# Kernel optimization log

Hardware: AMD Instinct MI355X
Metric: run time of the kernel (lower is better)

The kernel has to match this reference:

```python
import jax, jax.numpy as jnp
import numpy as np

DIM_V, DIM_T, DIM_OUT, NUM_HEADS = 1024, 1024, 1024, 16
HEAD_DIM = DIM_OUT // NUM_HEADS
BETA = 1.0  # module multiplies scores by self.beta (=1); self.scale is unused


def setup_inputs() -> dict:
    key = jax.random.key(0)
    ks = jax.random.split(key, 12)
    B, N1, N2 = 8, 256, 4096
    E = jax.random.normal(ks[0], (B, N1, DIM_T), dtype=jnp.float32)
    I = jax.random.normal(ks[1], (B, N2, DIM_V), dtype=jnp.float32)
    s = 0.02
    # Conv1d(kernel_size=1) == linear; weights stored [out, in], bias [out]
    q_w = jax.random.normal(ks[2], (DIM_OUT, DIM_T), dtype=jnp.float32) * s
    q_b = jnp.zeros((DIM_OUT,), dtype=jnp.float32)
    k_w = jax.random.normal(ks[3], (DIM_OUT, DIM_V), dtype=jnp.float32) * s
    k_b = jnp.zeros((DIM_OUT,), dtype=jnp.float32)
    v_w = jax.random.normal(ks[4], (DIM_OUT, DIM_V), dtype=jnp.float32) * s
    v_b = jnp.zeros((DIM_OUT,), dtype=jnp.float32)
    p_w = jax.random.normal(ks[5], (DIM_OUT, DIM_OUT), dtype=jnp.float32) * s
    p_b = jnp.zeros((DIM_OUT,), dtype=jnp.float32)
    return {"E": E, "I": I, "q_w": q_w, "q_b": q_b, "k_w": k_w, "k_b": k_b,
            "v_w": v_w, "v_b": v_b, "p_w": p_w, "p_b": p_b}


def reference(E, I, q_w, q_b, k_w, k_b, v_w, v_b, p_w, p_b):
    B, N1, _ = E.shape
    _, N2, _ = I.shape
    # 1x1 conv projections == dense layers over channel dim
    Q = (jnp.einsum('bnc,oc->bno', E, q_w) + q_b).reshape(B, N1, NUM_HEADS, HEAD_DIM)
    K = (jnp.einsum('bmc,oc->bmo', I, k_w) + k_b).reshape(B, N2, NUM_HEADS, HEAD_DIM)
    V = (jnp.einsum('bmc,oc->bmo', I, v_w) + v_b).reshape(B, N2, NUM_HEADS, HEAD_DIM)
    # cross-attention scores [B, H, N1, N2]
    attn = jnp.einsum('bnhd,bmhd->bhnm', Q, K) * BETA
    attn = jax.nn.softmax(attn, axis=-1)
    U = jnp.einsum('bhnm,bmhd->bnhd', attn, V).reshape(B, N1, DIM_OUT)
    U = jnp.einsum('bnc,oc->bno', U, p_w) + p_b
    U = U / jnp.linalg.norm(U, axis=-1, keepdims=True)
    return jnp.concatenate([E, U], axis=2)  # [B, N1, dim_t + dim_out]
```

## Files before the change

### kernel.cpp

```cpp
#include <hip/hip_runtime.h>
#include <hip/hip_bf16.h>
#include <stdint.h>


typedef __bf16 bf16_t;
typedef __attribute__((ext_vector_type(8))) __bf16 bf16x8;
typedef __attribute__((ext_vector_type(4))) float f32x4;

#define DEVINL __device__ __forceinline__

DEVINL f32x4 mfma16(bf16x8 a, bf16x8 b, f32x4 c) {
  return __builtin_amdgcn_mfma_f32_16x16x32_bf16(a, b, c, 0, 0, 0);
}

DEVINL bf16x8 load8(const bf16_t* p) { return *(const bf16x8*)p; }
DEVINL bf16x8 load8(const float* p) {
  const float4 u = *(const float4*)p;
  const float4 v = *(const float4*)(p + 4);
  bf16x8 r;
  r[0] = (bf16_t)u.x; r[1] = (bf16_t)u.y; r[2] = (bf16_t)u.z; r[3] = (bf16_t)u.w;
  r[4] = (bf16_t)v.x; r[5] = (bf16_t)v.y; r[6] = (bf16_t)v.z; r[7] = (bf16_t)v.w;
  return r;
}

DEVINL uint32_t pack_bf16(float a, float b) {
  union { bf16_t h[2]; uint32_t u; } x;
  x.h[0] = (bf16_t)a; x.h[1] = (bf16_t)b;
  return x.u;
}

DEVINL void async16(const void* g, void* l) {
  typedef const __attribute__((address_space(1))) unsigned int* gp1;
  typedef __attribute__((address_space(3))) unsigned int* lp3;
  __builtin_amdgcn_global_load_lds((gp1)(uintptr_t)g,
                                   (lp3)(uint32_t)(uintptr_t)l, 16, 0, 0);
}

__global__ __launch_bounds__(256) void cvt_f32_bf16(
    const float* __restrict__ src, bf16_t* __restrict__ dst, int n8) {
  const int i = blockIdx.x * 256 + threadIdx.x;
  if (i < n8) *(bf16x8*)(dst + (size_t)i * 8) = load8(src + (size_t)i * 8);
}

template <int MODE>
__global__ __launch_bounds__(256) void gemm_bt_async(
    const bf16_t* __restrict__ A, const bf16_t* __restrict__ B,
    const float* __restrict__ bias, bf16_t* __restrict__ C,
    int M, int N, int K) {
  __shared__ bf16_t As[2][128 * 32];
  __shared__ bf16_t Bs[2][128 * 32];
  const int tid = threadIdx.x;
  const int w = tid >> 6, lane = tid & 63, quad = lane >> 4, l16 = lane & 15;
  const int bid = blockIdx.x;
  const int swz = (bid & 7) * (int)(gridDim.x >> 3) + (bid >> 3);
  const int big = swz >> 3, small = swz & 7;
  const int bm = 128 * (MODE == 1 ? small : big);
  const int bn = 128 * (MODE == 1 ? big : small);
  const int wm = (w & 1) * 64, wn = (w >> 1) * 64;
  const int srow = tid >> 2;
  const int sw8 = ((tid & 3) ^ (srow & 3)) * 8;

  const bf16_t* Ag0 = A + (size_t)(bm + srow) * K + sw8;
  const bf16_t* Ag1 = Ag0 + (size_t)64 * K;
  const bf16_t* Bg0 = B + (size_t)(bn + srow) * K + sw8;
  const bf16_t* Bg1 = Bg0 + (size_t)64 * K;

  f32x4 acc[4][4] = {};

  for (int k0 = 0; k0 < K; k0 += 64) {
    async16(Ag0 + k0, As[0] + tid * 8);
    async16(Ag1 + k0, As[0] + 64 * 32 + tid * 8);
    async16(Bg0 + k0, Bs[0] + tid * 8);
    async16(Bg1 + k0, Bs[0] + 64 * 32 + tid * 8);
    async16(Ag0 + k0 + 32, As[1] + tid * 8);
    async16(Ag1 + k0 + 32, As[1] + 64 * 32 + tid * 8);
    async16(Bg0 + k0 + 32, Bs[1] + tid * 8);
    async16(Bg1 + k0 + 32, Bs[1] + 64 * 32 + tid * 8);
    __syncthreads();
#pragma unroll
    for (int h = 0; h < 2; h++) {
      bf16x8 af[4], bfr[4];
#pragma unroll
      for (int mt = 0; mt < 4; mt++) {
        const int r = wm + mt * 16 + l16;
        af[mt] = *(const bf16x8*)(As[h] + r * 32 + ((quad ^ (r & 3)) * 8));
      }
#pragma unroll
      for (int nt = 0; nt < 4; nt++) {
        const int r = wn + nt * 16 + l16;
        bfr[nt] = *(const bf16x8*)(Bs[h] + r * 32 + ((quad ^ (r & 3)) * 8));
      }
#pragma unroll
      for (int mt = 0; mt < 4; mt++)
#pragma unroll
        for (int nt = 0; nt < 4; nt++)
          acc[mt][nt] = mfma16(af[mt], bfr[nt], acc[mt][nt]);
    }
    __syncthreads();
  }

#pragma unroll
  for (int mt = 0; mt < 4; mt++) {
#pragma unroll
    for (int nt = 0; nt < 4; nt++) {
      const int gm0 = bm + wm + mt * 16 + quad * 4;
      const int gn = bn + wn + nt * 16 + l16;
#pragma unroll
      for (int r = 0; r < 4; r++) {
        const int gm = gm0 + r;
        C[(size_t)gm * N + gn] =
            (bf16_t)(acc[mt][nt][r] + bias[MODE == 1 ? gm : gn]);
      }
    }
  }
}

template <int MODE, typename TA, typename TB>
__global__ __launch_bounds__(256) void gemm_bt_reg(
    const TA* __restrict__ A, const TB* __restrict__ B,
    const float* __restrict__ bias, void* __restrict__ Cv,
    int M, int N, int K) {
  __shared__ bf16_t As[128 * 32];
  __shared__ bf16_t Bs[128 * 32];
  const int tid = threadIdx.x;
  const int w = tid >> 6, lane = tid & 63, quad = lane >> 4, l16 = lane & 15;
  const int bm = blockIdx.x * 128, bn = blockIdx.y * 128;
  const int wm = (w & 1) * 64, wn = (w >> 1) * 64;
  const int srow = tid >> 2;
  const int swz = ((tid & 3) ^ (srow & 3)) * 8;

  const TA* Ag0 = A + (size_t)(bm + srow) * K + swz;
  const TA* Ag1 = Ag0 + (size_t)64 * K;
  const TB* Bg0 = B + (size_t)(bn + srow) * K + swz;
  const TB* Bg1 = Bg0 + (size_t)64 * K;
  bf16_t* Al0 = As + tid * 8;
  bf16_t* Al1 = As + 64 * 32 + tid * 8;
  bf16_t* Bl0 = Bs + tid * 8;
  bf16_t* Bl1 = Bs + 64 * 32 + tid * 8;

  f32x4 acc[4][4] = {};

  for (int k0 = 0; k0 < K; k0 += 32) {
    const bf16x8 a0 = load8(Ag0 + k0);
    const bf16x8 a1 = load8(Ag1 + k0);
    const bf16x8 b0 = load8(Bg0 + k0);
    const bf16x8 b1 = load8(Bg1 + k0);
    *(bf16x8*)Al0 = a0;
    *(bf16x8*)Al1 = a1;
    *(bf16x8*)Bl0 = b0;
    *(bf16x8*)Bl1 = b1;
    __syncthreads();
    bf16x8 af[4], bfr[4];
#pragma unroll
    for (int mt = 0; mt < 4; mt++) {
      const int r = wm + mt * 16 + l16;
      af[mt] = *(const bf16x8*)(As + r * 32 + ((quad ^ (r & 3)) * 8));
    }
#pragma unroll
    for (int nt = 0; nt < 4; nt++) {
      const int r = wn + nt * 16 + l16;
      bfr[nt] = *(const bf16x8*)(Bs + r * 32 + ((quad ^ (r & 3)) * 8));
    }
#pragma unroll
    for (int mt = 0; mt < 4; mt++)
#pragma unroll
      for (int nt = 0; nt < 4; nt++)
        acc[mt][nt] = mfma16(af[mt], bfr[nt], acc[mt][nt]);
    __syncthreads();
  }

#pragma unroll
  for (int mt = 0; mt < 4; mt++) {
#pragma unroll
    for (int nt = 0; nt < 4; nt++) {
      const int gm0 = bm + wm + mt * 16 + quad * 4;
      const int gn = bn + wn + nt * 16 + l16;
#pragma unroll
      for (int r = 0; r < 4; r++) {
        const int gm = gm0 + r;
        float v = acc[mt][nt][r] + bias[MODE == 1 ? gm : gn];
        if (MODE == 2)
          ((float*)Cv)[(size_t)gm * N + gn] = v;
        else
          ((bf16_t*)Cv)[(size_t)gm * N + gn] = (bf16_t)v;
      }
    }
  }
}

__global__ __launch_bounds__(256) void attn_split(
    const bf16_t* __restrict__ QU, const bf16_t* __restrict__ Kbuf,
    const bf16_t* __restrict__ Vtbuf, float* __restrict__ opart,
    float* __restrict__ mls) {
  __shared__ bf16_t Ks[64 * 64];
  __shared__ bf16_t Vs[64 * 64];
  __shared__ bf16_t Ps[4][16 * 64];
  const int tid = threadIdx.x;
  const int w = tid >> 6, lane = tid & 63, quad = lane >> 4, l16 = lane & 15;
  const int flat = blockIdx.x;
  const int qt = flat >> 9, s = (flat >> 7) & 3, h = (flat >> 3) & 15, b = flat & 7;

  const int qlocal = qt * 64 + w * 16 + l16;
  const bf16_t* qbase = QU + (size_t)(b * 256 + qlocal) * 1024 + h * 64 + quad * 8;
  const bf16x8 qf0 = *(const bf16x8*)(qbase);
  const bf16x8 qf1 = *(const bf16x8*)(qbase + 32);

  const int srow = tid >> 3;
  const int swz = ((tid & 7) ^ (srow & 7)) * 8;
  const bf16_t* Kg =
      Kbuf + (size_t)(b * 4096 + s * 1024 + srow) * 1024 + h * 64 + swz;
  const bf16_t* Vg =
      Vtbuf + (size_t)(h * 64 + srow) * 32768 + b * 4096 + s * 1024 + swz;

  f32x4 o[4] = {};
  float m = -1e30f, l = 0.f;
  const float L2E = 1.4426950408889634f;

  bf16x8 kv0 = *(const bf16x8*)(Kg);
  bf16x8 kv1 = *(const bf16x8*)(Kg + (size_t)32 * 1024);
  bf16x8 vv0 = *(const bf16x8*)(Vg);
  bf16x8 vv1 = *(const bf16x8*)(Vg + (size_t)32 * 32768);

  for (int kt = 0; kt < 16; kt++) {
    __syncthreads();
    *(bf16x8*)(Ks + tid * 8) = kv0;
    *(bf16x8*)(Ks + 32 * 64 + tid * 8) = kv1;
    *(bf16x8*)(Vs + tid * 8) = vv0;
    *(bf16x8*)(Vs + 32 * 64 + tid * 8) = vv1;
    __syncthreads();
    if (kt < 15) {
      const size_t ko = (size_t)(kt + 1) * 64;
      kv0 = *(const bf16x8*)(Kg + ko * 1024);
      kv1 = *(const bf16x8*)(Kg + (ko + 32) * 1024);
      vv0 = *(const bf16x8*)(Vg + ko);
      vv1 = *(const bf16x8*)(Vg + ko + (size_t)32 * 32768);
    }

    f32x4 st[4];
#pragma unroll
    for (int nt = 0; nt < 4; nt++) {
      const int key = nt * 16 + l16;
      const bf16x8 kf0 = *(const bf16x8*)(Ks + key * 64 + ((quad ^ (key & 7)) * 8));
      const bf16x8 kf1 = *(const bf16x8*)(Ks + key * 64 + (((quad + 4) ^ (key & 7)) * 8));
      f32x4 z = {0.f, 0.f, 0.f, 0.f};
      z = mfma16(kf0, qf0, z);
      st[nt] = mfma16(kf1, qf1, z);
    }

    float mx = st[0][0];
#pragma unroll
    for (int nt = 0; nt < 4; nt++)
#pragma unroll
      for (int r = 0; r < 4; r++) mx = fmaxf(mx, st[nt][r]);
    mx = fmaxf(mx, __shfl_xor(mx, 16));
    mx = fmaxf(mx, __shfl_xor(mx, 32));
    const float mnew = fmaxf(m, mx);
    const float alpha = exp2f((m - mnew) * L2E);

    float rs = 0.f;
#pragma unroll
    for (int nt = 0; nt < 4; nt++) {
      const float p0 = exp2f((st[nt][0] - mnew) * L2E);
      const float p1 = exp2f((st[nt][1] - mnew) * L2E);
      const float p2 = exp2f((st[nt][2] - mnew) * L2E);
      const float p3 = exp2f((st[nt][3] - mnew) * L2E);
      rs += (p0 + p1) + (p2 + p3);
      uint2 pkv;
      pkv.x = pack_bf16(p0, p1);
      pkv.y = pack_bf16(p2, p3);
      *(uint2*)(&Ps[w][l16 * 64 + (((nt * 4 + quad) ^ l16) * 4)]) = pkv;
    }
    rs += __shfl_xor(rs, 16);
    rs += __shfl_xor(rs, 32);
    l = l * alpha + rs;
    m = mnew;
#pragma unroll
    for (int dt = 0; dt < 4; dt++) {
      o[dt][0] *= alpha; o[dt][1] *= alpha;
      o[dt][2] *= alpha; o[dt][3] *= alpha;
    }

#pragma unroll
    for (int ck = 0; ck < 2; ck++) {
      const int c0 = ck * 8 + quad * 2;
      union { uint2 ab[2]; bf16x8 v; } pf;
      pf.ab[0] = *(const uint2*)(&Ps[w][l16 * 64 + ((c0 ^ l16) * 4)]);
      pf.ab[1] = *(const uint2*)(&Ps[w][l16 * 64 + (((c0 + 1) ^ l16) * 4)]);
#pragma unroll
      for (int dt = 0; dt < 4; dt++) {
        const int row = dt * 16 + l16;
        const bf16x8 vf = *(const bf16x8*)(
            Vs + row * 64 + (((ck * 4 + quad) ^ (row & 7)) * 8));
        o[dt] = mfma16(vf, pf.v, o[dt]);
      }
    }
  }

  const int pr = ((b * 16 + h) << 8) | qlocal;
  if (quad == 0) {
    mls[((size_t)s * 32768 + pr) * 2 + 0] = m;
    mls[((size_t)s * 32768 + pr) * 2 + 1] = l;
  }
#pragma unroll
  for (int dt = 0; dt < 4; dt++)
    *(f32x4*)(opart + ((size_t)s * 32768 + pr) * 64 + dt * 16 + quad * 4) = o[dt];
}

__global__ __launch_bounds__(256) void attn_combine(
    const float* __restrict__ opart, const float* __restrict__ mls,
    bf16_t* __restrict__ QU) {
  const int w = threadIdx.x >> 6, lane = threadIdx.x & 63;
  const int pr = blockIdx.x * 4 + w;
  const float L2E = 1.4426950408889634f;
  float ms[4], ls[4];
#pragma unroll
  for (int s = 0; s < 4; s++) {
    ms[s] = mls[((size_t)s * 32768 + pr) * 2 + 0];
    ls[s] = mls[((size_t)s * 32768 + pr) * 2 + 1];
  }
  const float M = fmaxf(fmaxf(ms[0], ms[1]), fmaxf(ms[2], ms[3]));
  float L = 0.f, acc = 0.f;
#pragma unroll
  for (int s = 0; s < 4; s++) {
    const float e = exp2f((ms[s] - M) * L2E);
    L += ls[s] * e;
    acc += e * opart[((size_t)s * 32768 + pr) * 64 + lane];
  }
  const int b = pr >> 12, h = (pr >> 8) & 15, q = pr & 255;
  QU[(size_t)(b * 256 + q) * 1024 + h * 64 + lane] =
      (bf16_t)(acc / fmaxf(L, 1e-30f));
}

__global__ __launch_bounds__(256) void attn_old(
    bf16_t* QU, const bf16_t* __restrict__ Kbuf,
    const bf16_t* __restrict__ Vtbuf, int hg, int G, int Kst) {
  __shared__ bf16_t Ks[64 * 64];
  __shared__ bf16_t Vs[64 * 64];
  __shared__ bf16_t Ps[4][16 * 64];
  const int tid = threadIdx.x;
  const int w = tid >> 6, lane = tid & 63, quad = lane >> 4, l16 = lane & 15;
  const int flat = blockIdx.x;
  const int qt = flat / (8 * G);
  const int rem = flat - qt * 8 * G;
  const int hh = rem % G, b = rem / G;
  const int h = hg + hh;

  const int qrow = b * 256 + qt * 64 + w * 16 + l16;
  const bf16_t* qbase = QU + (size_t)qrow * 1024 + h * 64 + quad * 8;
  const bf16x8 qf0 = *(const bf16x8*)(qbase);
  const bf16x8 qf1 = *(const bf16x8*)(qbase + 32);

  const int srow = tid >> 3;
  const int swz = ((tid & 7) ^ (srow & 7)) * 8;
  const bf16_t* Kg = Kbuf + (size_t)(b * 4096 + srow) * Kst + hh * 64 + swz;
  const bf16_t* Vg = Vtbuf + (size_t)(hh * 64 + srow) * 32768 + b * 4096 + swz;

  f32x4 o[4] = {};
  float mrow[4] = {-1e30f, -1e30f, -1e30f, -1e30f};
  float lrow[4] = {0.f, 0.f, 0.f, 0.f};
  const float L2E = 1.4426950408889634f;

  bf16x8 kv0 = *(const bf16x8*)(Kg);
  bf16x8 kv1 = *(const bf16x8*)(Kg + (size_t)32 * Kst);
  bf16x8 vv0 = *(const bf16x8*)(Vg);
  bf16x8 vv1 = *(const bf16x8*)(Vg + (size_t)32 * 32768);

  for (int kt = 0; kt < 64; kt++) {
    __syncthreads();
    *(bf16x8*)(Ks + tid * 8) = kv0;
    *(bf16x8*)(Ks + 32 * 64 + tid * 8) = kv1;
    *(bf16x8*)(Vs + tid * 8) = vv0;
    *(bf16x8*)(Vs + 32 * 64 + tid * 8) = vv1;
    __syncthreads();
    if (kt < 63) {
      const size_t ko = (size_t)(kt + 1) * 64;
      kv0 = *(const bf16x8*)(Kg + ko * Kst);
      kv1 = *(const bf16x8*)(Kg + (ko + 32) * Kst);
      vv0 = *(const bf16x8*)(Vg + ko);
      vv1 = *(const bf16x8*)(Vg + ko + (size_t)32 * 32768);
    }

    f32x4 s[4];
#pragma unroll
    for (int nt = 0; nt < 4; nt++) {
      const int key = nt * 16 + l16;
      const bf16x8 kf0 = *(const bf16x8*)(Ks + key * 64 + ((quad ^ (key & 7)) * 8));
      const bf16x8 kf1 = *(const bf16x8*)(Ks + key * 64 + (((quad + 4) ^ (key & 7)) * 8));
      f32x4 z = {0.f, 0.f, 0.f, 0.f};
      z = mfma16(qf0, kf0, z);
      s[nt] = mfma16(qf1, kf1, z);
    }

    float mnew[4], alpha[4], rsum[4];
#pragma unroll
    for (int r = 0; r < 4; r++) {
      float mx = fmaxf(fmaxf(s[0][r], s[1][r]), fmaxf(s[2][r], s[3][r]));
      mx = fmaxf(mx, __shfl_xor(mx, 1));
      mx = fmaxf(mx, __shfl_xor(mx, 2));
      mx = fmaxf(mx, __shfl_xor(mx, 4));
      mx = fmaxf(mx, __shfl_xor(mx, 8));
      mnew[r] = fmaxf(mrow[r], mx);
      alpha[r] = exp2f((mrow[r] - mnew[r]) * L2E);
      rsum[r] = 0.f;
    }
#pragma unroll
    for (int nt = 0; nt < 4; nt++) {
      const int key = nt * 16 + l16;
#pragma unroll
      for (int r = 0; r < 4; r++) {
        const float p = exp2f((s[nt][r] - mnew[r]) * L2E);
        rsum[r] += p;
        const int q = quad * 4 + r;
        Ps[w][q * 64 + (((key >> 3) ^ (q & 7)) * 8) + (key & 7)] = (bf16_t)p;
      }
    }
#pragma unroll
    for (int r = 0; r < 4; r++) {
      rsum[r] += __shfl_xor(rsum[r], 1);
      rsum[r] += __shfl_xor(rsum[r], 2);
      rsum[r] += __shfl_xor(rsum[r], 4);
      rsum[r] += __shfl_xor(rsum[r], 8);
      lrow[r] = lrow[r] * alpha[r] + rsum[r];
      mrow[r] = mnew[r];
    }
#pragma unroll
    for (int nt = 0; nt < 4; nt++) {
      o[nt][0] *= alpha[0]; o[nt][1] *= alpha[1];
      o[nt][2] *= alpha[2]; o[nt][3] *= alpha[3];
    }

    __syncthreads();

    const bf16x8 pf0 = *(const bf16x8*)(&Ps[w][l16 * 64 + ((quad ^ (l16 & 7)) * 8)]);
    const bf16x8 pf1 = *(const bf16x8*)(&Ps[w][l16 * 64 + (((quad + 4) ^ (l16 & 7)) * 8)]);
#pragma unroll
    for (int nt = 0; nt < 4; nt++) {
      const int d = nt * 16 + l16;
      const bf16x8 vf0 = *(const bf16x8*)(Vs + d * 64 + ((quad ^ (d & 7)) * 8));
      const bf16x8 vf1 = *(const bf16x8*)(Vs + d * 64 + (((quad + 4) ^ (d & 7)) * 8));
      o[nt] = mfma16(pf0, vf0, o[nt]);
      o[nt] = mfma16(pf1, vf1, o[nt]);
    }
  }

  float inv[4];
#pragma unroll
  for (int r = 0; r < 4; r++) inv[r] = 1.0f / fmaxf(lrow[r], 1e-30f);
#pragma unroll
  for (int nt = 0; nt < 4; nt++) {
#pragma unroll
    for (int r = 0; r < 4; r++) {
      const int row = b * 256 + qt * 64 + w * 16 + quad * 4 + r;
      QU[(size_t)row * 1024 + h * 64 + nt * 16 + l16] = (bf16_t)(o[nt][r] * inv[r]);
    }
  }
}

__global__ __launch_bounds__(256) void norm_concat(
    const float* __restrict__ E, const float* __restrict__ P,
    float* __restrict__ out) {
  const int row = blockIdx.x, tid = threadIdx.x;
  const int w = tid >> 6, lane = tid & 63;

  *(float4*)(out + (size_t)row * 2048 + tid * 4) =
      *(const float4*)(E + (size_t)row * 1024 + tid * 4);

  const float4 p = *(const float4*)(P + (size_t)row * 1024 + tid * 4);
  float ss = p.x * p.x + p.y * p.y + p.z * p.z + p.w * p.w;
#pragma unroll
  for (int m = 1; m <= 32; m <<= 1) ss += __shfl_xor(ss, m);
  __shared__ float red[4];
  if (lane == 0) red[w] = ss;
  __syncthreads();
  const float rn = rsqrtf(fmaxf(red[0] + red[1] + red[2] + red[3], 1e-30f));
  float4 q;
  q.x = p.x * rn; q.y = p.y * rn; q.z = p.z * rn; q.w = p.w * rn;
  *(float4*)(out + (size_t)row * 2048 + 1024 + tid * 4) = q;
}

extern "C" void kernel_launch(void* const* d_in, const int* in_sizes, int n_in,
                              void* d_out, int out_size, void* d_ws, size_t ws_size,
                              hipStream_t stream) {
  (void)in_sizes; (void)n_in; (void)out_size;
  const float* E   = (const float*)d_in[0];
  const float* I   = (const float*)d_in[1];
  const float* q_w = (const float*)d_in[2];
  const float* q_b = (const float*)d_in[3];
  const float* k_w = (const float*)d_in[4];
  const float* k_b = (const float*)d_in[5];
  const float* v_w = (const float*)d_in[6];
  const float* v_b = (const float*)d_in[7];
  const float* p_w = (const float*)d_in[8];
  const float* p_b = (const float*)d_in[9];
  float* out = (float*)d_out;
  char* ws = (char*)d_ws;

  if (ws_size >= (200ull << 20)) {
    bf16_t* QU    = (bf16_t*)(ws);
    bf16_t* k_wbf = (bf16_t*)(ws + (4u << 20));
    bf16_t* v_wbf = (bf16_t*)(ws + (6u << 20));
    bf16_t* Ibf   = (bf16_t*)(ws + (8u << 20));
    float*  Pf    = (float*)(ws + (8u << 20));
    float*  opart = (float*)(ws + (16u << 20));
    float*  mls   = (float*)(ws + (52u << 20));
    bf16_t* Kbuf  = (bf16_t*)(ws + (72u << 20));
    bf16_t* Vtbuf = (bf16_t*)(ws + (136u << 20));

    cvt_f32_bf16<<<16384, 256, 0, stream>>>(I, Ibf, 32768 * 1024 / 8);
    cvt_f32_bf16<<<512, 256, 0, stream>>>(k_w, k_wbf, 1024 * 1024 / 8);
    cvt_f32_bf16<<<512, 256, 0, stream>>>(v_w, v_wbf, 1024 * 1024 / 8);

    gemm_bt_reg<0, float, float><<<dim3(16, 8), 256, 0, stream>>>(
        E, q_w, q_b, QU, 2048, 1024, 1024);
    gemm_bt_async<0><<<2048, 256, 0, stream>>>(
        Ibf, k_wbf, k_b, Kbuf, 32768, 1024, 1024);
    gemm_bt_async<1><<<2048, 256, 0, stream>>>(
        v_wbf, Ibf, v_b, Vtbuf, 1024, 32768, 1024);
    attn_split<<<2048, 256, 0, stream>>>(QU, Kbuf, Vtbuf, opart, mls);
    attn_combine<<<8192, 256, 0, stream>>>(opart, mls, QU);
    gemm_bt_reg<2, bf16_t, float><<<dim3(16, 8), 256, 0, stream>>>(
        QU, p_w, p_b, Pf, 2048, 1024, 1024);
    norm_concat<<<2048, 256, 0, stream>>>(E, Pf, out);
  } else {
    int G = 2;
    if (ws_size >= (133ull << 20)) G = 16;
    else if (ws_size >= (69ull << 20)) G = 8;
    else if (ws_size >= (37ull << 20)) G = 4;
    bf16_t* QU    = (bf16_t*)(ws);
    bf16_t* Kbuf  = (bf16_t*)(ws + (4u << 20));
    bf16_t* Vtbuf = (bf16_t*)(ws + (4u << 20) + ((size_t)G << 22));
    float*  Pf    = (float*)(ws + (4u << 20));

    gemm_bt_reg<0, float, float><<<dim3(16, 8), 256, 0, stream>>>(
        E, q_w, q_b, QU, 2048, 1024, 1024);
    for (int hg = 0; hg < 16; hg += G) {
      const int Nh = G * 64;
      gemm_bt_reg<0, float, float><<<dim3(256, Nh / 128), 256, 0, stream>>>(
          I, k_w + (size_t)hg * 64 * 1024, k_b + hg * 64, Kbuf, 32768, Nh, 1024);
      gemm_bt_reg<1, float, float><<<dim3(Nh / 128, 256), 256, 0, stream>>>(
          v_w + (size_t)hg * 64 * 1024, I, v_b + hg * 64, Vtbuf, Nh, 32768, 1024);
      attn_old<<<32 * G, 256, 0, stream>>>(QU, Kbuf, Vtbuf, hg, G, Nh);
    }
    gemm_bt_reg<2, bf16_t, float><<<dim3(16, 8), 256, 0, stream>>>(
        QU, p_w, p_b, Pf, 2048, 1024, 1024);
    norm_concat<<<2048, 256, 0, stream>>>(E, Pf, out);
  }
}
```

Baseline: 580.5 us.

## Rewrite split attention to keep K/V in registers with lazy softmax rescale

Replaces the LDS-staged attention kernel with one where each block handles 128 queries. Each wave loads its K and V fragments straight from global memory into registers, and a pair of waves splits the keys, merging their partial results through shared memory at the end. It also folds log2(e) into the Q projection epilogue, so exponentials become plain exp2. It skips the running-max rescale unless the max grows by more than 8. This removes LDS staging, barriers and per-tile multiplies, at the cost of uncoalesced strided global loads and higher register pressure.

```diff
diff --git a/kernel.cpp b/kernel.cpp
--- a/kernel.cpp
+++ b/kernel.cpp
@@ -5,6 +5,7 @@
 
 typedef __bf16 bf16_t;
 typedef __attribute__((ext_vector_type(8))) __bf16 bf16x8;
+typedef __attribute__((ext_vector_type(4))) __bf16 bf16x4;
 typedef __attribute__((ext_vector_type(4))) float f32x4;
 
 #define DEVINL __device__ __forceinline__
@@ -12,6 +13,8 @@
 DEVINL f32x4 mfma16(bf16x8 a, bf16x8 b, f32x4 c) {
   return __builtin_amdgcn_mfma_f32_16x16x32_bf16(a, b, c, 0, 0, 0);
 }
+
+DEVINL float fexp2(float x) { return __builtin_exp2f(x); }
 
 DEVINL bf16x8 load8(const bf16_t* p) { return *(const bf16x8*)p; }
 DEVINL bf16x8 load8(const float* p) {
@@ -179,6 +182,7 @@
       for (int r = 0; r < 4; r++) {
         const int gm = gm0 + r;
         float v = acc[mt][nt][r] + bias[MODE == 1 ? gm : gn];
+        if (MODE == 3) v *= 1.4426950408889634f;
         if (MODE == 2)
           ((float*)Cv)[(size_t)gm * N + gn] = v;
         else
@@ -188,122 +192,152 @@
   }
 }
 
-__global__ __launch_bounds__(256) void attn_split(
+__global__ __launch_bounds__(256) void attn_regs(
     const bf16_t* __restrict__ QU, const bf16_t* __restrict__ Kbuf,
     const bf16_t* __restrict__ Vtbuf, float* __restrict__ opart,
     float* __restrict__ mls) {
-  __shared__ bf16_t Ks[64 * 64];
-  __shared__ bf16_t Vs[64 * 64];
-  __shared__ bf16_t Ps[4][16 * 64];
+  __shared__ float lo[128 * 68];
+  __shared__ float lmx[2][128], ll[2][128];
   const int tid = threadIdx.x;
   const int w = tid >> 6, lane = tid & 63, quad = lane >> 4, l16 = lane & 15;
+  const int wq = w >> 1, wk = w & 1;
   const int flat = blockIdx.x;
   const int qt = flat >> 9, s = (flat >> 7) & 3, h = (flat >> 3) & 15, b = flat & 7;
 
-  const int qlocal = qt * 64 + w * 16 + l16;
-  const bf16_t* qbase = QU + (size_t)(b * 256 + qlocal) * 1024 + h * 64 + quad * 8;
-  const bf16x8 qf0 = *(const bf16x8*)(qbase);
-  const bf16x8 qf1 = *(const bf16x8*)(qbase + 32);
-
-  const int srow = tid >> 3;
-  const int swz = ((tid & 7) ^ (srow & 7)) * 8;
-  const bf16_t* Kg =
-      Kbuf + (size_t)(b * 4096 + s * 1024 + srow) * 1024 + h * 64 + swz;
-  const bf16_t* Vg =
-      Vtbuf + (size_t)(h * 64 + srow) * 32768 + b * 4096 + s * 1024 + swz;
-
-  f32x4 o[4] = {};
-  float m = -1e30f, l = 0.f;
-  const float L2E = 1.4426950408889634f;
-
-  bf16x8 kv0 = *(const bf16x8*)(Kg);
-  bf16x8 kv1 = *(const bf16x8*)(Kg + (size_t)32 * 1024);
-  bf16x8 vv0 = *(const bf16x8*)(Vg);
-  bf16x8 vv1 = *(const bf16x8*)(Vg + (size_t)32 * 32768);
-
-  for (int kt = 0; kt < 16; kt++) {
-    __syncthreads();
-    *(bf16x8*)(Ks + tid * 8) = kv0;
-    *(bf16x8*)(Ks + 32 * 64 + tid * 8) = kv1;
-    *(bf16x8*)(Vs + tid * 8) = vv0;
-    *(bf16x8*)(Vs + 32 * 64 + tid * 8) = vv1;
-    __syncthreads();
-    if (kt < 15) {
-      const size_t ko = (size_t)(kt + 1) * 64;
-      kv0 = *(const bf16x8*)(Kg + ko * 1024);
-      kv1 = *(const bf16x8*)(Kg + (ko + 32) * 1024);
-      vv0 = *(const bf16x8*)(Vg + ko);
-      vv1 = *(const bf16x8*)(Vg + ko + (size_t)32 * 32768);
-    }
-
-    f32x4 st[4];
-#pragma unroll
-    for (int nt = 0; nt < 4; nt++) {
-      const int key = nt * 16 + l16;
-      const bf16x8 kf0 = *(const bf16x8*)(Ks + key * 64 + ((quad ^ (key & 7)) * 8));
-      const bf16x8 kf1 = *(const bf16x8*)(Ks + key * 64 + (((quad + 4) ^ (key & 7)) * 8));
-      f32x4 z = {0.f, 0.f, 0.f, 0.f};
-      z = mfma16(kf0, qf0, z);
-      st[nt] = mfma16(kf1, qf1, z);
-    }
-
-    float mx = st[0][0];
-#pragma unroll
-    for (int nt = 0; nt < 4; nt++)
-#pragma unroll
-      for (int r = 0; r < 4; r++) mx = fmaxf(mx, st[nt][r]);
-    mx = fmaxf(mx, __shfl_xor(mx, 16));
-    mx = fmaxf(mx, __shfl_xor(mx, 32));
-    const float mnew = fmaxf(m, mx);
-    const float alpha = exp2f((m - mnew) * L2E);
-
-    float rs = 0.f;
-#pragma unroll
-    for (int nt = 0; nt < 4; nt++) {
-      const float p0 = exp2f((st[nt][0] - mnew) * L2E);
-      const float p1 = exp2f((st[nt][1] - mnew) * L2E);
-      const float p2 = exp2f((st[nt][2] - mnew) * L2E);
-      const float p3 = exp2f((st[nt][3] - mnew) * L2E);
-      rs += (p0 + p1) + (p2 + p3);
-      uint2 pkv;
-      pkv.x = pack_bf16(p0, p1);
-      pkv.y = pack_bf16(p2, p3);
-      *(uint2*)(&Ps[w][l16 * 64 + (((nt * 4 + quad) ^ l16) * 4)]) = pkv;
-    }
-    rs += __shfl_xor(rs, 16);
-    rs += __shfl_xor(rs, 32);
-    l = l * alpha + rs;
-    m = mnew;
+  bf16x8 qf0[4], qf1[4];
+  const bf16_t* qb =
+      QU + (size_t)(b * 256 + qt * 128 + wq * 64 + l16) * 1024 + h * 64 + quad * 8;
+#pragma unroll
+  for (int qg = 0; qg < 4; qg++) {
+    qf0[qg] = *(const bf16x8*)(qb + (size_t)qg * 16 * 1024);
+    qf1[qg] = *(const bf16x8*)(qb + (size_t)qg * 16 * 1024 + 32);
+  }
+
+  const bf16_t* kg =
+      Kbuf + (size_t)(b * 4096 + s * 1024 + wk * 32 + l16) * 1024 + h * 64 + quad * 8;
+  const bf16_t* vg =
+      Vtbuf + (size_t)(h * 64 + l16) * 32768 + b * 4096 + s * 1024 + wk * 32 + quad * 4;
+
+  f32x4 o[4][4] = {};
+  float m[4] = {-1e30f, -1e30f, -1e30f, -1e30f};
+  float l[4] = {};
+
+#pragma unroll 1
+  for (int it = 0; it < 16; it++) {
+    const bf16x8 kfe0 = *(const bf16x8*)(kg);
+    const bf16x8 kfe1 = *(const bf16x8*)(kg + 32);
+    const bf16x8 kfo0 = *(const bf16x8*)(kg + 16 * 1024);
+    const bf16x8 kfo1 = *(const bf16x8*)(kg + 16 * 1024 + 32);
+    bf16x8 vf[4];
 #pragma unroll
     for (int dt = 0; dt < 4; dt++) {
-      o[dt][0] *= alpha; o[dt][1] *= alpha;
-      o[dt][2] *= alpha; o[dt][3] *= alpha;
-    }
-
-#pragma unroll
-    for (int ck = 0; ck < 2; ck++) {
-      const int c0 = ck * 8 + quad * 2;
-      union { uint2 ab[2]; bf16x8 v; } pf;
-      pf.ab[0] = *(const uint2*)(&Ps[w][l16 * 64 + ((c0 ^ l16) * 4)]);
-      pf.ab[1] = *(const uint2*)(&Ps[w][l16 * 64 + (((c0 + 1) ^ l16) * 4)]);
+      union { bf16x4 h4[2]; bf16x8 v; } u;
+      u.h4[0] = *(const bf16x4*)(vg + (size_t)dt * 16 * 32768);
+      u.h4[1] = *(const bf16x4*)(vg + (size_t)dt * 16 * 32768 + 16);
+      vf[dt] = u.v;
+    }
+
+#pragma unroll
+    for (int qg = 0; qg < 4; qg++) {
+      f32x4 z0 = {};
+      z0 = mfma16(kfe0, qf0[qg], z0);
+      const f32x4 ste = mfma16(kfe1, qf1[qg], z0);
+      f32x4 z1 = {};
+      z1 = mfma16(kfo0, qf0[qg], z1);
+      const f32x4 sto = mfma16(kfo1, qf1[qg], z1);
+
+      float mx = fmaxf(fmaxf(ste[0], ste[1]), fmaxf(ste[2], ste[3]));
+      mx = fmaxf(mx, fmaxf(fmaxf(sto[0], sto[1]), fmaxf(sto[2], sto[3])));
+      mx = fmaxf(mx, __shfl_xor(mx, 16));
+      mx = fmaxf(mx, __shfl_xor(mx, 32));
+
+      if (!__all(mx <= m[qg] + 8.f)) {
+        const float mn = fmaxf(m[qg], mx);
+        const float al = fexp2(m[qg] - mn);
+        m[qg] = mn;
+        l[qg] *= al;
+#pragma unroll
+        for (int dt = 0; dt < 4; dt++) {
+          o[dt][qg][0] *= al; o[dt][qg][1] *= al;
+          o[dt][qg][2] *= al; o[dt][qg][3] *= al;
+        }
+      }
+      const float mq = m[qg];
+      float pe[4], po[4];
+#pragma unroll
+      for (int r = 0; r < 4; r++) {
+        pe[r] = fexp2(ste[r] - mq);
+        po[r] = fexp2(sto[r] - mq);
+      }
+      float rs = ((pe[0] + pe[1]) + (pe[2] + pe[3])) +
+                 ((po[0] + po[1]) + (po[2] + po[3]));
+      rs += __shfl_xor(rs, 16);
+      rs += __shfl_xor(rs, 32);
+      l[qg] += rs;
+
+      union { uint32_t u[4]; bf16x8 v; } pb;
+      pb.u[0] = pack_bf16(pe[0], pe[1]);
+      pb.u[1] = pack_bf16(pe[2], pe[3]);
+      pb.u[2] = pack_bf16(po[0], po[1]);
+      pb.u[3] = pack_bf16(po[2], po[3]);
+#pragma unroll
+      for (int dt = 0; dt < 4; dt++)
+        o[dt][qg] = mfma16(vf[dt], pb.v, o[dt][qg]);
+    }
+    kg += 64 * 1024;
+    vg += 64;
+  }
+
+  if (quad == 0) {
+#pragma unroll
+    for (int qg = 0; qg < 4; qg++) {
+      const int q = wq * 64 + qg * 16 + l16;
+      lmx[wk][q] = m[qg];
+      ll[wk][q] = l[qg];
+    }
+  }
+  __syncthreads();
+  float sc[4], Mq[4];
+#pragma unroll
+  for (int qg = 0; qg < 4; qg++) {
+    const int q = wq * 64 + qg * 16 + l16;
+    Mq[qg] = fmaxf(lmx[0][q], lmx[1][q]);
+    sc[qg] = fexp2(m[qg] - Mq[qg]);
+#pragma unroll
+    for (int dt = 0; dt < 4; dt++) {
+      o[dt][qg][0] *= sc[qg]; o[dt][qg][1] *= sc[qg];
+      o[dt][qg][2] *= sc[qg]; o[dt][qg][3] *= sc[qg];
+    }
+  }
+  if (wk == 0) {
+#pragma unroll
+    for (int qg = 0; qg < 4; qg++)
+#pragma unroll
+      for (int dt = 0; dt < 4; dt++)
+        *(f32x4*)&lo[(wq * 64 + qg * 16 + l16) * 68 + dt * 16 + quad * 4] =
+            o[dt][qg];
+  }
+  __syncthreads();
+  if (wk == 1) {
+    const int pr0 = ((b * 16 + h) << 8) | (qt * 128 + wq * 64);
+#pragma unroll
+    for (int qg = 0; qg < 4; qg++) {
+      const int q = wq * 64 + qg * 16 + l16;
+      const int pr = pr0 + qg * 16 + l16;
 #pragma unroll
       for (int dt = 0; dt < 4; dt++) {
-        const int row = dt * 16 + l16;
-        const bf16x8 vf = *(const bf16x8*)(
-            Vs + row * 64 + (((ck * 4 + quad) ^ (row & 7)) * 8));
-        o[dt] = mfma16(vf, pf.v, o[dt]);
-      }
-    }
-  }
-
-  const int pr = ((b * 16 + h) << 8) | qlocal;
-  if (quad == 0) {
-    mls[((size_t)s * 32768 + pr) * 2 + 0] = m;
-    mls[((size_t)s * 32768 + pr) * 2 + 1] = l;
-  }
-#pragma unroll
-  for (int dt = 0; dt < 4; dt++)
-    *(f32x4*)(opart + ((size_t)s * 32768 + pr) * 64 + dt * 16 + quad * 4) = o[dt];
+        f32x4 t = *(const f32x4*)&lo[q * 68 + dt * 16 + quad * 4];
+        t = t + o[dt][qg];
+        *(f32x4*)(opart + ((size_t)s * 32768 + pr) * 64 + dt * 16 + quad * 4) = t;
+      }
+      if (quad == 0) {
+        const float L =
+            ll[0][q] * fexp2(lmx[0][q] - Mq[qg]) + l[qg] * sc[qg];
+        mls[((size_t)s * 32768 + pr) * 2 + 0] = Mq[qg];
+        mls[((size_t)s * 32768 + pr) * 2 + 1] = L;
+      }
+    }
+  }
 }
 
 __global__ __launch_bounds__(256) void attn_combine(
@@ -311,7 +345,6 @@
     bf16_t* __restrict__ QU) {
   const int w = threadIdx.x >> 6, lane = threadIdx.x & 63;
   const int pr = blockIdx.x * 4 + w;
-  const float L2E = 1.4426950408889634f;
   float ms[4], ls[4];
 #pragma unroll
   for (int s = 0; s < 4; s++) {
@@ -322,7 +355,7 @@
   float L = 0.f, acc = 0.f;
 #pragma unroll
   for (int s = 0; s < 4; s++) {
-    const float e = exp2f((ms[s] - M) * L2E);
+    const float e = fexp2(ms[s] - M);
     L += ls[s] * e;
     acc += e * opart[((size_t)s * 32768 + pr) * 64 + lane];
   }
@@ -510,13 +543,13 @@
     cvt_f32_bf16<<<512, 256, 0, stream>>>(k_w, k_wbf, 1024 * 1024 / 8);
     cvt_f32_bf16<<<512, 256, 0, stream>>>(v_w, v_wbf, 1024 * 1024 / 8);
 
-    gemm_bt_reg<0, float, float><<<dim3(16, 8), 256, 0, stream>>>(
+    gemm_bt_reg<3, float, float><<<dim3(16, 8), 256, 0, stream>>>(
         E, q_w, q_b, QU, 2048, 1024, 1024);
     gemm_bt_async<0><<<2048, 256, 0, stream>>>(
         Ibf, k_wbf, k_b, Kbuf, 32768, 1024, 1024);
     gemm_bt_async<1><<<2048, 256, 0, stream>>>(
         v_wbf, Ibf, v_b, Vtbuf, 1024, 32768, 1024);
-    attn_split<<<2048, 256, 0, stream>>>(QU, Kbuf, Vtbuf, opart, mls);
+    attn_regs<<<1024, 256, 0, stream>>>(QU, Kbuf, Vtbuf, opart, mls);
     attn_combine<<<8192, 256, 0, stream>>>(opart, mls, QU);
     gemm_bt_reg<2, bf16_t, float><<<dim3(16, 8), 256, 0, stream>>>(
         QU, p_w, p_b, Pf, 2048, 1024, 1024);
```

Result: slower. 592.3 us (+2.0%).
